# Optimization experiments

Measured on AMD Instinct MI355X. Metric: run time of the kernel, lower is better.

The kernel has to match this reference:

```python
import jax, jax.numpy as jnp
from jax import lax
import numpy as np

B, N = 8, 8192
NPOINT, RADIUS, NSAMPLE = 2048, 0.4, 64
EPS = 1e-5


def setup_inputs() -> dict:
    key = jax.random.key(0)
    ks = jax.random.split(key, 8)
    d = {
        'xyz': jax.random.normal(ks[0], (B, N, 3), jnp.float32),
        'features': jax.random.normal(ks[1], (B, 64, N), jnp.float32),
        'W0': jax.random.normal(ks[2], (64, 67), jnp.float32) * 0.1,
        'g0': jnp.ones((64,), jnp.float32), 'b0': jnp.zeros((64,), jnp.float32),
        'm0': jnp.zeros((64,), jnp.float32), 'v0': jnp.ones((64,), jnp.float32),
        'W1': jax.random.normal(ks[3], (64, 64), jnp.float32) * 0.1,
        'g1': jnp.ones((64,), jnp.float32), 'b1': jnp.zeros((64,), jnp.float32),
        'm1': jnp.zeros((64,), jnp.float32), 'v1': jnp.ones((64,), jnp.float32),
        'W2': jax.random.normal(ks[4], (128, 64), jnp.float32) * 0.1,
        'g2': jnp.ones((128,), jnp.float32), 'b2': jnp.zeros((128,), jnp.float32),
        'm2': jnp.zeros((128,), jnp.float32), 'v2': jnp.ones((128,), jnp.float32),
    }
    return d


def fps(xyz, npoint):
    # sequential furthest point sampling, start at index 0 (as in CUDA op)
    b = xyz.shape[0]
    first = jnp.zeros((b,), jnp.int32)
    d0 = jnp.sum((xyz - xyz[:, :1]) ** 2, -1)  # (B,N) dist to point 0

    def body(dist, _):
        nxt = jnp.argmax(dist, -1).astype(jnp.int32)
        p = jnp.take_along_axis(xyz, nxt[:, None, None].astype(jnp.int32), axis=1)
        dist = jnp.minimum(dist, jnp.sum((xyz - p) ** 2, -1))
        return dist, nxt

    _, rest = lax.scan(body, d0, None, length=npoint - 1)  # rest: (npoint-1, B)
    return jnp.concatenate([first[:, None], rest.T], axis=1)  # (B, npoint)


def ball_query(xyz, new_xyz, radius, nsample):
    # (B,P,N) squared distances
    d2 = jnp.sum((new_xyz[:, :, None, :] - xyz[:, None, :, :]) ** 2, -1)
    mask = d2 < radius * radius
    # stable sort: in-radius indices first, in original order (matches CUDA fill order)
    order = jnp.argsort(jnp.where(mask, 0, 1).astype(jnp.int32), axis=-1, stable=True)
    idx = order[..., :nsample]
    cnt = jnp.sum(mask, -1)  # (B,P)
    pos = jnp.arange(nsample)
    return jnp.where(pos < cnt[..., None], idx, idx[..., :1])  # pad with first found


def group(x, idx):
    # x (B,N,D), idx (B,P,S) -> (B,P,S,D)
    return jnp.take_along_axis(x[:, None], idx[..., None], axis=2)


def reference(xyz, features, W0, g0, b0, m0, v0, W1, g1, b1, m1, v1, W2, g2, b2, m2, v2):
    inds = fps(xyz, NPOINT)                                   # (B,P)
    new_xyz = jnp.take_along_axis(xyz, inds[..., None], axis=1)  # (B,P,3)
    idx = ball_query(xyz, new_xyz, RADIUS, NSAMPLE)           # (B,P,S)
    gxyz = group(xyz, idx) - new_xyz[:, :, None, :]           # (B,P,S,3) centered
    gfeat = group(jnp.swapaxes(features, 1, 2), idx)          # (B,P,S,C)
    x = jnp.concatenate([gxyz, gfeat], -1)                    # use_xyz concat
    x = jnp.transpose(x, (0, 3, 1, 2))                        # (B,C+3,P,S)
    for W, g, b, m, v in ((W0, g0, b0, m0, v0), (W1, g1, b1, m1, v1), (W2, g2, b2, m2, v2)):
        x = jnp.einsum('oi,bips->bops', W, x)                 # 1x1 conv
        scale = g / jnp.sqrt(v + EPS)
        x = (x - m[:, None, None]) * scale[:, None, None] + b[:, None, None]
        x = jax.nn.relu(x)
    new_features = jnp.max(x, -1)                             # max pool over nsample -> (B,128,P)
    return new_xyz, new_features, inds
```

## Files before the change

### kernel.cpp

```cpp
#include <hip/hip_runtime.h>
#include <cstdint>
#include <cstddef>

#define BATCH   8
#define NPTS    8192
#define NPOINT  2048
#define NSAMPLE 64
#define K0      67
#define C2      128

__device__ __forceinline__ float d2e(float ax, float ay, float az,
                                     float bx, float by, float bz) {
#pragma clang fp contract(off)
  float dx = ax - bx;
  float dy = ay - by;
  float dz = az - bz;
  float t0 = dx * dx;
  float t1 = dy * dy;
  float t2 = dz * dz;
  return (t0 + t1) + t2;
}

__device__ __forceinline__ float dpp_max_f32(float x) {
  int v;
  v = __builtin_amdgcn_update_dpp(__float_as_int(x), __float_as_int(x), 0xB1, 0xF, 0xF, false);
  x = fmaxf(x, __int_as_float(v));
  v = __builtin_amdgcn_update_dpp(__float_as_int(x), __float_as_int(x), 0x4E, 0xF, 0xF, false);
  x = fmaxf(x, __int_as_float(v));
  v = __builtin_amdgcn_update_dpp(__float_as_int(x), __float_as_int(x), 0x141, 0xF, 0xF, false);
  x = fmaxf(x, __int_as_float(v));
  v = __builtin_amdgcn_update_dpp(__float_as_int(x), __float_as_int(x), 0x140, 0xF, 0xF, false);
  x = fmaxf(x, __int_as_float(v));
  v = __builtin_amdgcn_update_dpp(__float_as_int(x), __float_as_int(x), 0x142, 0xA, 0xF, false);
  x = fmaxf(x, __int_as_float(v));
  v = __builtin_amdgcn_update_dpp(__float_as_int(x), __float_as_int(x), 0x143, 0xC, 0xF, false);
  x = fmaxf(x, __int_as_float(v));
  return __int_as_float(__builtin_amdgcn_readlane(__float_as_int(x), 63));
}

__device__ __forceinline__ int dpp_min_i32(int x) {
  int v;
  v = __builtin_amdgcn_update_dpp(x, x, 0xB1, 0xF, 0xF, false); x = min(x, v);
  v = __builtin_amdgcn_update_dpp(x, x, 0x4E, 0xF, 0xF, false); x = min(x, v);
  v = __builtin_amdgcn_update_dpp(x, x, 0x141, 0xF, 0xF, false); x = min(x, v);
  v = __builtin_amdgcn_update_dpp(x, x, 0x140, 0xF, 0xF, false); x = min(x, v);
  v = __builtin_amdgcn_update_dpp(x, x, 0x142, 0xA, 0xF, false); x = min(x, v);
  v = __builtin_amdgcn_update_dpp(x, x, 0x143, 0xC, 0xF, false); x = min(x, v);
  return __builtin_amdgcn_readlane(x, 63);
}

__global__ __launch_bounds__(512) void fps_kernel(const float* __restrict__ xyz,
                                                  float* __restrict__ out_xyz,
                                                  float* __restrict__ out_inds) {
  const int b = blockIdx.x;
  const int tid = threadIdx.x;
  const int lane = tid & 63, w = tid >> 6;

  __shared__ float2 sxy[NPTS];
  __shared__ float  szl[NPTS];
  __shared__ unsigned short sslot[NPOINT];
  __shared__ unsigned long long wred[2][8] __attribute__((aligned(16)));

  const float* xb = xyz + (size_t)b * NPTS * 3;

  for (int k = 0; k < 16; k++) {
    int i = tid + k * 512;
    sxy[i] = make_float2(xb[i * 3 + 0], xb[i * 3 + 1]);
    szl[i] = xb[i * 3 + 2];
  }
  __syncthreads();

  const float2 q0xy = sxy[0];
  const float q0x = q0xy.x, q0y = q0xy.y, q0z = szl[0];

  const int base = tid * 16;
  float px[16], py[16], pz[16], dd[16];
#pragma unroll
  for (int j = 0; j < 16; j++) {
    float2 xy = sxy[base + j];
    px[j] = xy.x; py[j] = xy.y; pz[j] = szl[base + j];
    dd[j] = d2e(px[j], py[j], pz[j], q0x, q0y, q0z);
  }
  if (tid == 0) sslot[0] = 0;

  {
    float bv = dd[0]; int bj = base;
#pragma unroll
    for (int j = 1; j < 16; j++) {
      bool better = dd[j] > bv;
      bv = better ? dd[j] : bv;
      bj = better ? base + j : bj;
    }
    float vm = dpp_max_f32(bv);
    int ci = (bv == vm) ? bj : 0x7FFFFFFF;
    int widx = dpp_min_i32(ci);
    if (lane == 0)
      wred[0][w] = ((unsigned long long)(~__float_as_uint(vm)) << 32) | (unsigned)widx;
  }
  __syncthreads();

  for (int t = 1; t < NPOINT; ++t) {
    const ulonglong2* wv = (const ulonglong2*)wred[(t - 1) & 1];
    ulonglong2 p0 = wv[0], p1 = wv[1], p2 = wv[2], p3 = wv[3];
    unsigned long long g0 = (p0.y < p0.x) ? p0.y : p0.x;
    unsigned long long g1 = (p1.y < p1.x) ? p1.y : p1.x;
    unsigned long long g2 = (p2.y < p2.x) ? p2.y : p2.x;
    unsigned long long g3 = (p3.y < p3.x) ? p3.y : p3.x;
    g0 = (g1 < g0) ? g1 : g0; g2 = (g3 < g2) ? g3 : g2;
    g0 = (g2 < g0) ? g2 : g0;
    const int nxt = (int)(g0 & 0xFFFFFFFFu);
    const float2 qxy = sxy[nxt];
    const float qx = qxy.x, qy = qxy.y, qz = szl[nxt];
    if (tid == 0) sslot[t] = (unsigned short)nxt;

    float d0 = d2e(px[0], py[0], pz[0], qx, qy, qz);
    dd[0] = fminf(dd[0], d0);
    float bv = dd[0]; int bj = base;
#pragma unroll
    for (int j = 1; j < 16; j++) {
      float d = d2e(px[j], py[j], pz[j], qx, qy, qz);
      dd[j] = fminf(dd[j], d);
      bool better = dd[j] > bv;
      bv = better ? dd[j] : bv;
      bj = better ? base + j : bj;
    }
    float vm = dpp_max_f32(bv);
    int ci = (bv == vm) ? bj : 0x7FFFFFFF;
    int widx = dpp_min_i32(ci);
    if (lane == 0)
      wred[t & 1][w] = ((unsigned long long)(~__float_as_uint(vm)) << 32) | (unsigned)widx;
    __syncthreads();
  }

  for (int t = tid; t < NPOINT; t += 512) {
    int o = (int)sslot[t];
    float2 xy = sxy[o];
    out_inds[b * NPOINT + t] = (float)o;
    out_xyz[((size_t)b * NPOINT + t) * 3 + 0] = xy.x;
    out_xyz[((size_t)b * NPOINT + t) * 3 + 1] = xy.y;
    out_xyz[((size_t)b * NPOINT + t) * 3 + 2] = szl[o];
  }
}

__global__ __launch_bounds__(128) void prep_kernel(
    const float* __restrict__ W0, const float* __restrict__ g0,
    const float* __restrict__ b0, const float* __restrict__ m0,
    const float* __restrict__ v0, const float* __restrict__ g1,
    const float* __restrict__ b1, const float* __restrict__ m1,
    const float* __restrict__ v1, const float* __restrict__ g2,
    const float* __restrict__ b2, const float* __restrict__ m2,
    const float* __restrict__ v2, float* __restrict__ wsp) {
  const int tid = threadIdx.x;
  if (tid < 64) {
    float s0 = g0[tid] / sqrtf(v0[tid] + 1e-5f);
    wsp[4 * tid + 0] = s0 * W0[tid * K0 + 0];
    wsp[4 * tid + 1] = s0 * W0[tid * K0 + 1];
    wsp[4 * tid + 2] = s0 * W0[tid * K0 + 2];
    wsp[4 * tid + 3] = b0[tid] - m0[tid] * s0;
    wsp[640 + tid] = s0;
    float s1 = g1[tid] / sqrtf(v1[tid] + 1e-5f);
    wsp[256 + tid] = s1; wsp[320 + tid] = b1[tid] - m1[tid] * s1;
  }
  float s2 = g2[tid] / sqrtf(v2[tid] + 1e-5f);
  wsp[384 + tid] = s2; wsp[512 + tid] = b2[tid] - m2[tid] * s2;
}

__global__ __launch_bounds__(256) void zfeat_kernel(const float* __restrict__ xyz,
                                                    const float* __restrict__ feat,
                                                    const float* __restrict__ W0,
                                                    const float* __restrict__ wsp,
                                                    float* __restrict__ szp) {
  __shared__ float ftile[64][64];
  __shared__ float sxyz[192];
  const int bt = blockIdx.x;
  const int b = bt >> 7, nt = bt & 127;
  const int tid = threadIdx.x;
  const int lane = tid & 63, w = tid >> 6;

  const float* fb = feat + (size_t)b * 64 * NPTS + (size_t)nt * 64;
#pragma unroll
  for (int r = w; r < 64; r += 4)
    ftile[r][lane] = fb[(size_t)r * NPTS + lane];
  if (tid < 192)
    sxyz[tid] = xyz[((size_t)b * NPTS + (size_t)nt * 64) * 3 + tid];

  float w0x = W0[lane * K0 + 0], w0y = W0[lane * K0 + 1], w0z = W0[lane * K0 + 2];
  float wf[64];
#pragma unroll
  for (int i = 0; i < 64; i++) wf[i] = W0[lane * K0 + 3 + i];
  const float s0 = wsp[640 + lane];
  __syncthreads();

  float* ob = szp + ((size_t)b * NPTS + (size_t)nt * 64) * 64;
  for (int u = w; u < 64; u += 4) {
    float acc = w0x * sxyz[u * 3 + 0] + w0y * sxyz[u * 3 + 1] + w0z * sxyz[u * 3 + 2];
#pragma unroll
    for (int i = 0; i < 64; i++) acc = fmaf(wf[i], ftile[i][u], acc);
    ob[(size_t)u * 64 + lane] = acc * s0;
  }
}

__global__ __launch_bounds__(256) void ballq_kernel(const float* __restrict__ xyz,
                                                    const float* __restrict__ new_xyz,
                                                    int* __restrict__ ball) {
  const int lane = threadIdx.x & 63;
  const int q = blockIdx.x * 4 + (threadIdx.x >> 6);
  const int b = q >> 11;
  const float RR = (float)(0.4 * 0.4);
  const float cx = new_xyz[(size_t)q * 3 + 0];
  const float cy = new_xyz[(size_t)q * 3 + 1];
  const float cz = new_xyz[(size_t)q * 3 + 2];
  const float* xb = xyz + (size_t)b * NPTS * 3;
  int cnt = 0, firsti = -1;
  for (int base = 0; base < NPTS; base += 64) {
    int i = base + lane;
    float xx = xb[i * 3 + 0], yy = xb[i * 3 + 1], zz = xb[i * 3 + 2];
    float d2 = d2e(xx, yy, zz, cx, cy, cz);
    bool m = d2 < RR;
    unsigned long long mask = __ballot(m);
    if (mask) {
      if (firsti < 0) firsti = base + (__ffsll((unsigned long long)mask) - 1);
      int pos = cnt + (int)__popcll(mask & ((1ull << lane) - 1ull));
      if (m && pos < NSAMPLE) ball[(size_t)q * NSAMPLE + pos] = i;
      cnt += (int)__popcll(mask);
      if (cnt >= NSAMPLE) break;
    }
  }
  for (int s = cnt + lane; s < NSAMPLE; s += 64)
    ball[(size_t)q * NSAMPLE + s] = firsti;
}

#define QPW 4
__global__ __launch_bounds__(256, 2) void mlp_kernel(
    const float* __restrict__ szp, const int* __restrict__ ball,
    const float* __restrict__ new_xyz, const float* __restrict__ W1,
    const float* __restrict__ W2, const float* __restrict__ wsp,
    float* __restrict__ out_feat) {
  __shared__ float ylds[4][2][64];
  __shared__ int   blds[4][64];
  const int tid = threadIdx.x;
  const int lane = tid & 63, wid = tid >> 6;

  float4 w1v[16], w2av[16], w2bv[16];
  const float4* W1r = (const float4*)(W1 + lane * 64);
  const float4* W2ar = (const float4*)(W2 + lane * 64);
  const float4* W2br = (const float4*)(W2 + (lane + 64) * 64);
#pragma unroll
  for (int i = 0; i < 16; i++) { w1v[i] = W1r[i]; w2av[i] = W2ar[i]; w2bv[i] = W2br[i]; }
  const float4 A = ((const float4*)wsp)[lane];
  const float sc1l = wsp[256 + lane], sh1l = wsp[320 + lane];
  const float sc2al = wsp[384 + lane], sh2al = wsp[512 + lane];
  const float sc2bl = wsp[448 + lane], sh2bl = wsp[576 + lane];

  float* yA = ylds[wid][0];
  float* yB = ylds[wid][1];
  const float4* yva = (const float4*)yA;
  const float4* yvb = (const float4*)yB;

  for (int qi = 0; qi < QPW; qi++) {
    const int q = blockIdx.x * (4 * QPW) + qi * 4 + wid;
    const int b = q >> 11, p = q & 2047;

    const float cx = new_xyz[(size_t)q * 3 + 0];
    const float cy = new_xyz[(size_t)q * 3 + 1];
    const float cz = new_xyz[(size_t)q * 3 + 2];
    const float hc = A.w - (A.x * cx + A.y * cy + A.z * cz);

    blds[wid][lane] = ball[(size_t)q * NSAMPLE + lane];
    const float* szb = szp + (size_t)b * NPTS * 64;
    __builtin_amdgcn_s_waitcnt(0);

    float vA = 0.f, vB = 0.f;
    int i0 = blds[wid][0], i1 = blds[wid][1];
    float fA = szb[(size_t)i0 * 64 + lane];
    float fB = szb[(size_t)i1 * 64 + lane];

    for (int s = 0; s < NSAMPLE; s += 2) {
      int sn0 = (s + 2 < NSAMPLE) ? s + 2 : s;
      int sn1 = (s + 3 < NSAMPLE) ? s + 3 : s;
      int in0 = blds[wid][sn0], in1 = blds[wid][sn1];
      float fn0 = szb[(size_t)in0 * 64 + lane];
      float fn1 = szb[(size_t)in1 * 64 + lane];

      float y0a = fmaxf(fA + hc, 0.f);
      float y0b = fmaxf(fB + hc, 0.f);
      yA[lane] = y0a;
      yB[lane] = y0b;
      float a0 = 0.f, a1 = 0.f, b0_ = 0.f, b1_ = 0.f;
#pragma unroll
      for (int i = 0; i < 16; i++) {
        float4 ya = yva[i], yb = yvb[i];
        float4 wv = w1v[i];
        a0 = fmaf(wv.x, ya.x, a0); a1 = fmaf(wv.y, ya.y, a1);
        a0 = fmaf(wv.z, ya.z, a0); a1 = fmaf(wv.w, ya.w, a1);
        b0_ = fmaf(wv.x, yb.x, b0_); b1_ = fmaf(wv.y, yb.y, b1_);
        b0_ = fmaf(wv.z, yb.z, b0_); b1_ = fmaf(wv.w, yb.w, b1_);
      }
      float y1a = fmaxf(fmaf(a0 + a1, sc1l, sh1l), 0.f);
      float y1b = fmaxf(fmaf(b0_ + b1_, sc1l, sh1l), 0.f);
      yA[lane] = y1a;
      yB[lane] = y1b;
      float c0 = 0.f, c1 = 0.f, e0 = 0.f, e1 = 0.f;
      float c0b = 0.f, c1b = 0.f, e0b = 0.f, e1b = 0.f;
#pragma unroll
      for (int i = 0; i < 16; i++) {
        float4 ya = yva[i], yb = yvb[i];
        float4 wa = w2av[i], wb = w2bv[i];
        c0 = fmaf(wa.x, ya.x, c0); c1 = fmaf(wa.y, ya.y, c1);
        c0 = fmaf(wa.z, ya.z, c0); c1 = fmaf(wa.w, ya.w, c1);
        e0 = fmaf(wb.x, ya.x, e0); e1 = fmaf(wb.y, ya.y, e1);
        e0 = fmaf(wb.z, ya.z, e0); e1 = fmaf(wb.w, ya.w, e1);
        c0b = fmaf(wa.x, yb.x, c0b); c1b = fmaf(wa.y, yb.y, c1b);
        c0b = fmaf(wa.z, yb.z, c0b); c1b = fmaf(wa.w, yb.w, c1b);
        e0b = fmaf(wb.x, yb.x, e0b); e1b = fmaf(wb.y, yb.y, e1b);
        e0b = fmaf(wb.z, yb.z, e0b); e1b = fmaf(wb.w, yb.w, e1b);
      }
      float y2aA = fmaxf(fmaf(c0 + c1, sc2al, sh2al), 0.f);
      float y2bA = fmaxf(fmaf(e0 + e1, sc2bl, sh2bl), 0.f);
      float y2aB = fmaxf(fmaf(c0b + c1b, sc2al, sh2al), 0.f);
      float y2bB = fmaxf(fmaf(e0b + e1b, sc2bl, sh2bl), 0.f);
      vA = fmaxf(vA, fmaxf(y2aA, y2aB));
      vB = fmaxf(vB, fmaxf(y2bA, y2bB));
      fA = fn0;
      fB = fn1;
    }
    out_feat[((size_t)b * C2 + lane) * NPOINT + p] = vA;
    out_feat[((size_t)b * C2 + lane + 64) * NPOINT + p] = vB;
  }
}

extern "C" void kernel_launch(void* const* d_in, const int* in_sizes, int n_in,
                              void* d_out, int out_size, void* d_ws, size_t ws_size,
                              hipStream_t stream) {
  const float* xyz  = (const float*)d_in[0];
  const float* feat = (const float*)d_in[1];
  const float* W0 = (const float*)d_in[2];
  const float* g0 = (const float*)d_in[3];
  const float* b0 = (const float*)d_in[4];
  const float* m0 = (const float*)d_in[5];
  const float* v0 = (const float*)d_in[6];
  const float* W1 = (const float*)d_in[7];
  const float* g1 = (const float*)d_in[8];
  const float* b1 = (const float*)d_in[9];
  const float* m1 = (const float*)d_in[10];
  const float* v1 = (const float*)d_in[11];
  const float* W2 = (const float*)d_in[12];
  const float* g2 = (const float*)d_in[13];
  const float* b2 = (const float*)d_in[14];
  const float* m2 = (const float*)d_in[15];
  const float* v2 = (const float*)d_in[16];

  float* out = (float*)d_out;
  float* out_xyz  = out;
  float* out_feat = out + 49152;
  float* out_inds = out + 49152 + 2097152;

  int*   ball = (int*)d_ws;
  float* szp  = (float*)((char*)d_ws + 4194304);
  float* wsp  = (float*)((char*)d_ws + 20971520);

  hipLaunchKernelGGL(prep_kernel, dim3(1), dim3(128), 0, stream,
                     W0, g0, b0, m0, v0, g1, b1, m1, v1, g2, b2, m2, v2, wsp);
  hipLaunchKernelGGL(zfeat_kernel, dim3(BATCH * (NPTS / 64)), dim3(256), 0, stream,
                     xyz, feat, W0, wsp, szp);
  hipLaunchKernelGGL(fps_kernel, dim3(BATCH), dim3(512), 0, stream,
                     xyz, out_xyz, out_inds);
  hipLaunchKernelGGL(ballq_kernel, dim3((BATCH * NPOINT) / 4), dim3(256), 0, stream,
                     xyz, out_xyz, ball);
  hipLaunchKernelGGL(mlp_kernel, dim3((BATCH * NPOINT) / (4 * QPW)), dim3(256), 0, stream,
                     szp, ball, out_xyz, W1, W2, wsp, out_feat);
}
```

Measured before the change: 2.714 ms.

## Fuse FPS, feature projection, ball query and MLP into one persistent streaming kernel

```diff
diff --git a/kernel.cpp b/kernel.cpp
--- a/kernel.cpp
+++ b/kernel.cpp
@@ -49,96 +49,265 @@
   return __builtin_amdgcn_readlane(x, 63);
 }
 
-__global__ __launch_bounds__(512) void fps_kernel(const float* __restrict__ xyz,
-                                                  float* __restrict__ out_xyz,
-                                                  float* __restrict__ out_inds) {
-  const int b = blockIdx.x;
+__device__ __forceinline__ void st_rel(int* p, int v) {
+  __hip_atomic_store(p, v, __ATOMIC_RELEASE, __HIP_MEMORY_SCOPE_AGENT);
+}
+__device__ __forceinline__ int ld_acq(int* p) {
+  return __hip_atomic_load(p, __ATOMIC_ACQUIRE, __HIP_MEMORY_SCOPE_AGENT);
+}
+
+__global__ __launch_bounds__(512, 2) void mega_kernel(
+    const float* __restrict__ xyz, const float* __restrict__ feat,
+    const float* __restrict__ W0, const float* __restrict__ W1,
+    const float* __restrict__ W2, const float* __restrict__ wsp,
+    float* __restrict__ szp, int* __restrict__ ctr,
+    float* __restrict__ out_xyz, float* __restrict__ out_feat,
+    float* __restrict__ out_inds) {
   const int tid = threadIdx.x;
-  const int lane = tid & 63, w = tid >> 6;
-
-  __shared__ float2 sxy[NPTS];
-  __shared__ float  szl[NPTS];
-  __shared__ unsigned short sslot[NPOINT];
-  __shared__ unsigned long long wred[2][8] __attribute__((aligned(16)));
-
-  const float* xb = xyz + (size_t)b * NPTS * 3;
-
-  for (int k = 0; k < 16; k++) {
-    int i = tid + k * 512;
-    sxy[i] = make_float2(xb[i * 3 + 0], xb[i * 3 + 1]);
-    szl[i] = xb[i * 3 + 2];
+  const int lane = tid & 63;
+  int* prog = ctr;
+  int* zcnt = ctr + 8;
+
+  if (blockIdx.x < 8) {
+    const int b = blockIdx.x;
+    const int w = tid >> 6;
+    __shared__ float2 sxy[NPTS];
+    __shared__ float  szl[NPTS];
+    __shared__ unsigned long long wred[2][8] __attribute__((aligned(16)));
+
+    const float* xb = xyz + (size_t)b * NPTS * 3;
+    for (int k = 0; k < 16; k++) {
+      int i = tid + k * 512;
+      sxy[i] = make_float2(xb[i * 3 + 0], xb[i * 3 + 1]);
+      szl[i] = xb[i * 3 + 2];
+    }
+    __syncthreads();
+
+    const float2 q0xy = sxy[0];
+    const float q0x = q0xy.x, q0y = q0xy.y, q0z = szl[0];
+
+    const int base = tid * 16;
+    float px[16], py[16], pz[16], dd[16];
+#pragma unroll
+    for (int j = 0; j < 16; j++) {
+      float2 xy = sxy[base + j];
+      px[j] = xy.x; py[j] = xy.y; pz[j] = szl[base + j];
+      dd[j] = d2e(px[j], py[j], pz[j], q0x, q0y, q0z);
+    }
+    if (tid == 0) {
+      out_inds[b * NPOINT] = 0.f;
+      out_xyz[(size_t)b * NPOINT * 3 + 0] = q0x;
+      out_xyz[(size_t)b * NPOINT * 3 + 1] = q0y;
+      out_xyz[(size_t)b * NPOINT * 3 + 2] = q0z;
+    }
+    {
+      float bv = dd[0]; int bj = base;
+#pragma unroll
+      for (int j = 1; j < 16; j++) {
+        bool better = dd[j] > bv;
+        bv = better ? dd[j] : bv;
+        bj = better ? base + j : bj;
+      }
+      float vm = dpp_max_f32(bv);
+      int ci = (bv == vm) ? bj : 0x7FFFFFFF;
+      int widx = dpp_min_i32(ci);
+      if (lane == 0)
+        wred[0][w] = ((unsigned long long)(~__float_as_uint(vm)) << 32) | (unsigned)widx;
+    }
+    __syncthreads();
+
+    for (int t = 1; t < NPOINT; ++t) {
+      const ulonglong2* wv = (const ulonglong2*)wred[(t - 1) & 1];
+      ulonglong2 p0 = wv[0], p1 = wv[1], p2 = wv[2], p3 = wv[3];
+      unsigned long long g0 = (p0.y < p0.x) ? p0.y : p0.x;
+      unsigned long long g1 = (p1.y < p1.x) ? p1.y : p1.x;
+      unsigned long long g2 = (p2.y < p2.x) ? p2.y : p2.x;
+      unsigned long long g3 = (p3.y < p3.x) ? p3.y : p3.x;
+      g0 = (g1 < g0) ? g1 : g0; g2 = (g3 < g2) ? g3 : g2;
+      g0 = (g2 < g0) ? g2 : g0;
+      const int nxt = (int)(g0 & 0xFFFFFFFFu);
+      const float2 qxy = sxy[nxt];
+      const float qx = qxy.x, qy = qxy.y, qz = szl[nxt];
+      if (tid == 0) {
+        out_inds[b * NPOINT + t] = (float)nxt;
+        out_xyz[((size_t)b * NPOINT + t) * 3 + 0] = qx;
+        out_xyz[((size_t)b * NPOINT + t) * 3 + 1] = qy;
+        out_xyz[((size_t)b * NPOINT + t) * 3 + 2] = qz;
+        if ((t & 31) == 31) st_rel(&prog[b], t + 1);
+      }
+
+      float d0 = d2e(px[0], py[0], pz[0], qx, qy, qz);
+      dd[0] = fminf(dd[0], d0);
+      float bv = dd[0]; int bj = base;
+#pragma unroll
+      for (int j = 1; j < 16; j++) {
+        float d = d2e(px[j], py[j], pz[j], qx, qy, qz);
+        dd[j] = fminf(dd[j], d);
+        bool better = dd[j] > bv;
+        bv = better ? dd[j] : bv;
+        bj = better ? base + j : bj;
+      }
+      float vm = dpp_max_f32(bv);
+      int ci = (bv == vm) ? bj : 0x7FFFFFFF;
+      int widx = dpp_min_i32(ci);
+      if (lane == 0)
+        wred[t & 1][w] = ((unsigned long long)(~__float_as_uint(vm)) << 32) | (unsigned)widx;
+      __syncthreads();
+    }
+    return;
+  }
+
+  const int wb = blockIdx.x - 8;
+  const int w8 = tid >> 6;
+  __shared__ float ftile[64][64];
+  __shared__ float sxyzt[192];
+  __shared__ float ylds2[8][2][64];
+  __shared__ int   blds8[8][64];
+
+  for (int tt = 0; tt < 2; tt++) {
+    const int bt = wb * 2 + tt;
+    const int B = bt >> 7, nt = bt & 127;
+    const float* fb = feat + (size_t)B * 64 * NPTS + (size_t)nt * 64;
+    for (int r = w8; r < 64; r += 8)
+      ftile[r][lane] = fb[(size_t)r * NPTS + lane];
+    if (tid < 192)
+      sxyzt[tid] = xyz[((size_t)B * NPTS + (size_t)nt * 64) * 3 + tid];
+    float w0x = W0[lane * K0 + 0], w0y = W0[lane * K0 + 1], w0z = W0[lane * K0 + 2];
+    float wf[64];
+#pragma unroll
+    for (int i = 0; i < 64; i++) wf[i] = W0[lane * K0 + 3 + i];
+    const float s0 = wsp[640 + lane];
+    __syncthreads();
+    float* ob = szp + ((size_t)B * NPTS + (size_t)nt * 64) * 64;
+    for (int u = w8; u < 64; u += 8) {
+      float acc = w0x * sxyzt[u * 3 + 0] + w0y * sxyzt[u * 3 + 1] + w0z * sxyzt[u * 3 + 2];
+#pragma unroll
+      for (int i = 0; i < 64; i++) acc = fmaf(wf[i], ftile[i][u], acc);
+      ob[(size_t)u * 64 + lane] = acc * s0;
+    }
+    __syncthreads();
+    if (tid == 0) {
+      __threadfence();
+      __hip_atomic_fetch_add(&zcnt[B], 1, __ATOMIC_RELEASE, __HIP_MEMORY_SCOPE_AGENT);
+    }
+  }
+
+  const int B0 = wb >> 6;
+  {
+    int guard = 0;
+    while (ld_acq(&zcnt[B0]) < 128 && ++guard < (1 << 20))
+      __builtin_amdgcn_s_sleep(8);
   }
   __syncthreads();
 
-  const float2 q0xy = sxy[0];
-  const float q0x = q0xy.x, q0y = q0xy.y, q0z = szl[0];
-
-  const int base = tid * 16;
-  float px[16], py[16], pz[16], dd[16];
-#pragma unroll
-  for (int j = 0; j < 16; j++) {
-    float2 xy = sxy[base + j];
-    px[j] = xy.x; py[j] = xy.y; pz[j] = szl[base + j];
-    dd[j] = d2e(px[j], py[j], pz[j], q0x, q0y, q0z);
-  }
-  if (tid == 0) sslot[0] = 0;
-
-  {
-    float bv = dd[0]; int bj = base;
-#pragma unroll
-    for (int j = 1; j < 16; j++) {
-      bool better = dd[j] > bv;
-      bv = better ? dd[j] : bv;
-      bj = better ? base + j : bj;
-    }
-    float vm = dpp_max_f32(bv);
-    int ci = (bv == vm) ? bj : 0x7FFFFFFF;
-    int widx = dpp_min_i32(ci);
-    if (lane == 0)
-      wred[0][w] = ((unsigned long long)(~__float_as_uint(vm)) << 32) | (unsigned)widx;
-  }
-  __syncthreads();
-
-  for (int t = 1; t < NPOINT; ++t) {
-    const ulonglong2* wv = (const ulonglong2*)wred[(t - 1) & 1];
-    ulonglong2 p0 = wv[0], p1 = wv[1], p2 = wv[2], p3 = wv[3];
-    unsigned long long g0 = (p0.y < p0.x) ? p0.y : p0.x;
-    unsigned long long g1 = (p1.y < p1.x) ? p1.y : p1.x;
-    unsigned long long g2 = (p2.y < p2.x) ? p2.y : p2.x;
-    unsigned long long g3 = (p3.y < p3.x) ? p3.y : p3.x;
-    g0 = (g1 < g0) ? g1 : g0; g2 = (g3 < g2) ? g3 : g2;
-    g0 = (g2 < g0) ? g2 : g0;
-    const int nxt = (int)(g0 & 0xFFFFFFFFu);
-    const float2 qxy = sxy[nxt];
-    const float qx = qxy.x, qy = qxy.y, qz = szl[nxt];
-    if (tid == 0) sslot[t] = (unsigned short)nxt;
-
-    float d0 = d2e(px[0], py[0], pz[0], qx, qy, qz);
-    dd[0] = fminf(dd[0], d0);
-    float bv = dd[0]; int bj = base;
-#pragma unroll
-    for (int j = 1; j < 16; j++) {
-      float d = d2e(px[j], py[j], pz[j], qx, qy, qz);
-      dd[j] = fminf(dd[j], d);
-      bool better = dd[j] > bv;
-      bv = better ? dd[j] : bv;
-      bj = better ? base + j : bj;
-    }
-    float vm = dpp_max_f32(bv);
-    int ci = (bv == vm) ? bj : 0x7FFFFFFF;
-    int widx = dpp_min_i32(ci);
-    if (lane == 0)
-      wred[t & 1][w] = ((unsigned long long)(~__float_as_uint(vm)) << 32) | (unsigned)widx;
-    __syncthreads();
-  }
-
-  for (int t = tid; t < NPOINT; t += 512) {
-    int o = (int)sslot[t];
-    float2 xy = sxy[o];
-    out_inds[b * NPOINT + t] = (float)o;
-    out_xyz[((size_t)b * NPOINT + t) * 3 + 0] = xy.x;
-    out_xyz[((size_t)b * NPOINT + t) * 3 + 1] = xy.y;
-    out_xyz[((size_t)b * NPOINT + t) * 3 + 2] = szl[o];
+  float4 w1v[16], w2av[16], w2bv[16];
+  const float4* W1r = (const float4*)(W1 + lane * 64);
+  const float4* W2ar = (const float4*)(W2 + lane * 64);
+  const float4* W2br = (const float4*)(W2 + (lane + 64) * 64);
+#pragma unroll
+  for (int i = 0; i < 16; i++) { w1v[i] = W1r[i]; w2av[i] = W2ar[i]; w2bv[i] = W2br[i]; }
+  const float4 Aq = ((const float4*)wsp)[lane];
+  const float sc1l = wsp[256 + lane], sh1l = wsp[320 + lane];
+  const float sc2al = wsp[384 + lane], sh2al = wsp[512 + lane];
+  const float sc2bl = wsp[448 + lane], sh2bl = wsp[576 + lane];
+  const float RR = (float)(0.4 * 0.4);
+
+  float* yA = ylds2[w8][0];
+  float* yB = ylds2[w8][1];
+  const float4* yva = (const float4*)yA;
+  const float4* yvb = (const float4*)yB;
+  int* bl = blds8[w8];
+  const float* xb = xyz + (size_t)B0 * NPTS * 3;
+  const float* szb = szp + (size_t)B0 * NPTS * 64;
+
+  for (int qi = 0; qi < 4; qi++) {
+    const int q = wb * 32 + qi * 8 + w8;
+    const int p = q & 2047;
+
+    {
+      int guard = 0;
+      while (ld_acq(&prog[B0]) < p + 1 && ++guard < (1 << 20))
+        __builtin_amdgcn_s_sleep(8);
+    }
+    const float cx = out_xyz[(size_t)q * 3 + 0];
+    const float cy = out_xyz[(size_t)q * 3 + 1];
+    const float cz = out_xyz[(size_t)q * 3 + 2];
+    const float hc = Aq.w - (Aq.x * cx + Aq.y * cy + Aq.z * cz);
+
+    int cnt = 0, firsti = -1;
+    for (int base2 = 0; base2 < NPTS; base2 += 64) {
+      int i = base2 + lane;
+      float xx = xb[i * 3 + 0], yy = xb[i * 3 + 1], zz = xb[i * 3 + 2];
+      float dq = d2e(xx, yy, zz, cx, cy, cz);
+      bool m = dq < RR;
+      unsigned long long mask = __ballot(m);
+      if (mask) {
+        if (firsti < 0) firsti = base2 + (__ffsll((unsigned long long)mask) - 1);
+        int pos = cnt + (int)__popcll(mask & ((1ull << lane) - 1ull));
+        if (m && pos < NSAMPLE) bl[pos] = i;
+        cnt += (int)__popcll(mask);
+        if (cnt >= NSAMPLE) break;
+      }
+    }
+    for (int s = cnt + lane; s < NSAMPLE; s += 64) bl[s] = firsti;
+    __builtin_amdgcn_s_waitcnt(0);
+
+    float vA = 0.f, vB = 0.f;
+    int i0 = bl[0], i1 = bl[1];
+    float fA = szb[(size_t)i0 * 64 + lane];
+    float fB = szb[(size_t)i1 * 64 + lane];
+
+    for (int s = 0; s < NSAMPLE; s += 2) {
+      int sn0 = (s + 2 < NSAMPLE) ? s + 2 : s;
+      int sn1 = (s + 3 < NSAMPLE) ? s + 3 : s;
+      int in0 = bl[sn0], in1 = bl[sn1];
+      float fn0 = szb[(size_t)in0 * 64 + lane];
+      float fn1 = szb[(size_t)in1 * 64 + lane];
+
+      float y0a = fmaxf(fA + hc, 0.f);
+      float y0b = fmaxf(fB + hc, 0.f);
+      yA[lane] = y0a;
+      yB[lane] = y0b;
+      float a0 = 0.f, a1 = 0.f, b0_ = 0.f, b1_ = 0.f;
+#pragma unroll
+      for (int i = 0; i < 16; i++) {
+        float4 ya = yva[i], yb = yvb[i];
+        float4 wv = w1v[i];
+        a0 = fmaf(wv.x, ya.x, a0); a1 = fmaf(wv.y, ya.y, a1);
+        a0 = fmaf(wv.z, ya.z, a0); a1 = fmaf(wv.w, ya.w, a1);
+        b0_ = fmaf(wv.x, yb.x, b0_); b1_ = fmaf(wv.y, yb.y, b1_);
+        b0_ = fmaf(wv.z, yb.z, b0_); b1_ = fmaf(wv.w, yb.w, b1_);
+      }
+      float y1a = fmaxf(fmaf(a0 + a1, sc1l, sh1l), 0.f);
+      float y1b = fmaxf(fmaf(b0_ + b1_, sc1l, sh1l), 0.f);
+      yA[lane] = y1a;
+      yB[lane] = y1b;
+      float c0 = 0.f, c1 = 0.f, e0 = 0.f, e1 = 0.f;
+      float c0b = 0.f, c1b = 0.f, e0b = 0.f, e1b = 0.f;
+#pragma unroll
+      for (int i = 0; i < 16; i++) {
+        float4 ya = yva[i], yb = yvb[i];
+        float4 wa = w2av[i], wbv = w2bv[i];
+        c0 = fmaf(wa.x, ya.x, c0); c1 = fmaf(wa.y, ya.y, c1);
+        c0 = fmaf(wa.z, ya.z, c0); c1 = fmaf(wa.w, ya.w, c1);
+        e0 = fmaf(wbv.x, ya.x, e0); e1 = fmaf(wbv.y, ya.y, e1);
+        e0 = fmaf(wbv.z, ya.z, e0); e1 = fmaf(wbv.w, ya.w, e1);
+        c0b = fmaf(wa.x, yb.x, c0b); c1b = fmaf(wa.y, yb.y, c1b);
+        c0b = fmaf(wa.z, yb.z, c0b); c1b = fmaf(wa.w, yb.w, c1b);
+        e0b = fmaf(wbv.x, yb.x, e0b); e1b = fmaf(wbv.y, yb.y, e1b);
+        e0b = fmaf(wbv.z, yb.z, e0b); e1b = fmaf(wbv.w, yb.w, e1b);
+      }
+      float y2aA = fmaxf(fmaf(c0 + c1, sc2al, sh2al), 0.f);
+      float y2bA = fmaxf(fmaf(e0 + e1, sc2bl, sh2bl), 0.f);
+      float y2aB = fmaxf(fmaf(c0b + c1b, sc2al, sh2al), 0.f);
+      float y2bB = fmaxf(fmaf(e0b + e1b, sc2bl, sh2bl), 0.f);
+      vA = fmaxf(vA, fmaxf(y2aA, y2aB));
+      vB = fmaxf(vB, fmaxf(y2bA, y2bB));
+      fA = fn0;
+      fB = fn1;
+    }
+    out_feat[((size_t)B0 * C2 + lane) * NPOINT + p] = vA;
+    out_feat[((size_t)B0 * C2 + lane + 64) * NPOINT + p] = vB;
   }
 }
 
@@ -149,8 +318,10 @@
     const float* __restrict__ b1, const float* __restrict__ m1,
     const float* __restrict__ v1, const float* __restrict__ g2,
     const float* __restrict__ b2, const float* __restrict__ m2,
-    const float* __restrict__ v2, float* __restrict__ wsp) {
+    const float* __restrict__ v2, float* __restrict__ wsp,
+    int* __restrict__ ctr) {
   const int tid = threadIdx.x;
+  if (tid < 16) ctr[tid] = 0;
   if (tid < 64) {
     float s0 = g0[tid] / sqrtf(v0[tid] + 1e-5f);
     wsp[4 * tid + 0] = s0 * W0[tid * K0 + 0];
@@ -163,170 +334,6 @@
   }
   float s2 = g2[tid] / sqrtf(v2[tid] + 1e-5f);
   wsp[384 + tid] = s2; wsp[512 + tid] = b2[tid] - m2[tid] * s2;
-}
-
-__global__ __launch_bounds__(256) void zfeat_kernel(const float* __restrict__ xyz,
-                                                    const float* __restrict__ feat,
-                                                    const float* __restrict__ W0,
-                                                    const float* __restrict__ wsp,
-                                                    float* __restrict__ szp) {
-  __shared__ float ftile[64][64];
-  __shared__ float sxyz[192];
-  const int bt = blockIdx.x;
-  const int b = bt >> 7, nt = bt & 127;
-  const int tid = threadIdx.x;
-  const int lane = tid & 63, w = tid >> 6;
-
-  const float* fb = feat + (size_t)b * 64 * NPTS + (size_t)nt * 64;
-#pragma unroll
-  for (int r = w; r < 64; r += 4)
-    ftile[r][lane] = fb[(size_t)r * NPTS + lane];
-  if (tid < 192)
-    sxyz[tid] = xyz[((size_t)b * NPTS + (size_t)nt * 64) * 3 + tid];
-
-  float w0x = W0[lane * K0 + 0], w0y = W0[lane * K0 + 1], w0z = W0[lane * K0 + 2];
-  float wf[64];
-#pragma unroll
-  for (int i = 0; i < 64; i++) wf[i] = W0[lane * K0 + 3 + i];
-  const float s0 = wsp[640 + lane];
-  __syncthreads();
-
-  float* ob = szp + ((size_t)b * NPTS + (size_t)nt * 64) * 64;
-  for (int u = w; u < 64; u += 4) {
-    float acc = w0x * sxyz[u * 3 + 0] + w0y * sxyz[u * 3 + 1] + w0z * sxyz[u * 3 + 2];
-#pragma unroll
-    for (int i = 0; i < 64; i++) acc = fmaf(wf[i], ftile[i][u], acc);
-    ob[(size_t)u * 64 + lane] = acc * s0;
-  }
-}
-
-__global__ __launch_bounds__(256) void ballq_kernel(const float* __restrict__ xyz,
-                                                    const float* __restrict__ new_xyz,
-                                                    int* __restrict__ ball) {
-  const int lane = threadIdx.x & 63;
-  const int q = blockIdx.x * 4 + (threadIdx.x >> 6);
-  const int b = q >> 11;
-  const float RR = (float)(0.4 * 0.4);
-  const float cx = new_xyz[(size_t)q * 3 + 0];
-  const float cy = new_xyz[(size_t)q * 3 + 1];
-  const float cz = new_xyz[(size_t)q * 3 + 2];
-  const float* xb = xyz + (size_t)b * NPTS * 3;
-  int cnt = 0, firsti = -1;
-  for (int base = 0; base < NPTS; base += 64) {
-    int i = base + lane;
-    float xx = xb[i * 3 + 0], yy = xb[i * 3 + 1], zz = xb[i * 3 + 2];
-    float d2 = d2e(xx, yy, zz, cx, cy, cz);
-    bool m = d2 < RR;
-    unsigned long long mask = __ballot(m);
-    if (mask) {
-      if (firsti < 0) firsti = base + (__ffsll((unsigned long long)mask) - 1);
-      int pos = cnt + (int)__popcll(mask & ((1ull << lane) - 1ull));
-      if (m && pos < NSAMPLE) ball[(size_t)q * NSAMPLE + pos] = i;
-      cnt += (int)__popcll(mask);
-      if (cnt >= NSAMPLE) break;
-    }
-  }
-  for (int s = cnt + lane; s < NSAMPLE; s += 64)
-    ball[(size_t)q * NSAMPLE + s] = firsti;
-}
-
-#define QPW 4
-__global__ __launch_bounds__(256, 2) void mlp_kernel(
-    const float* __restrict__ szp, const int* __restrict__ ball,
-    const float* __restrict__ new_xyz, const float* __restrict__ W1,
-    const float* __restrict__ W2, const float* __restrict__ wsp,
-    float* __restrict__ out_feat) {
-  __shared__ float ylds[4][2][64];
-  __shared__ int   blds[4][64];
-  const int tid = threadIdx.x;
-  const int lane = tid & 63, wid = tid >> 6;
-
-  float4 w1v[16], w2av[16], w2bv[16];
-  const float4* W1r = (const float4*)(W1 + lane * 64);
-  const float4* W2ar = (const float4*)(W2 + lane * 64);
-  const float4* W2br = (const float4*)(W2 + (lane + 64) * 64);
-#pragma unroll
-  for (int i = 0; i < 16; i++) { w1v[i] = W1r[i]; w2av[i] = W2ar[i]; w2bv[i] = W2br[i]; }
-  const float4 A = ((const float4*)wsp)[lane];
-  const float sc1l = wsp[256 + lane], sh1l = wsp[320 + lane];
-  const float sc2al = wsp[384 + lane], sh2al = wsp[512 + lane];
-  const float sc2bl = wsp[448 + lane], sh2bl = wsp[576 + lane];
-
-  float* yA = ylds[wid][0];
-  float* yB = ylds[wid][1];
-  const float4* yva = (const float4*)yA;
-  const float4* yvb = (const float4*)yB;
-
-  for (int qi = 0; qi < QPW; qi++) {
-    const int q = blockIdx.x * (4 * QPW) + qi * 4 + wid;
-    const int b = q >> 11, p = q & 2047;
-
-    const float cx = new_xyz[(size_t)q * 3 + 0];
-    const float cy = new_xyz[(size_t)q * 3 + 1];
-    const float cz = new_xyz[(size_t)q * 3 + 2];
-    const float hc = A.w - (A.x * cx + A.y * cy + A.z * cz);
-
-    blds[wid][lane] = ball[(size_t)q * NSAMPLE + lane];
-    const float* szb = szp + (size_t)b * NPTS * 64;
-    __builtin_amdgcn_s_waitcnt(0);
-
-    float vA = 0.f, vB = 0.f;
-    int i0 = blds[wid][0], i1 = blds[wid][1];
-    float fA = szb[(size_t)i0 * 64 + lane];
-    float fB = szb[(size_t)i1 * 64 + lane];
-
-    for (int s = 0; s < NSAMPLE; s += 2) {
-      int sn0 = (s + 2 < NSAMPLE) ? s + 2 : s;
-      int sn1 = (s + 3 < NSAMPLE) ? s + 3 : s;
-      int in0 = blds[wid][sn0], in1 = blds[wid][sn1];
-      float fn0 = szb[(size_t)in0 * 64 + lane];
-      float fn1 = szb[(size_t)in1 * 64 + lane];
-
-      float y0a = fmaxf(fA + hc, 0.f);
-      float y0b = fmaxf(fB + hc, 0.f);
-      yA[lane] = y0a;
-      yB[lane] = y0b;
-      float a0 = 0.f, a1 = 0.f, b0_ = 0.f, b1_ = 0.f;
-#pragma unroll
-      for (int i = 0; i < 16; i++) {
-        float4 ya = yva[i], yb = yvb[i];
-        float4 wv = w1v[i];
-        a0 = fmaf(wv.x, ya.x, a0); a1 = fmaf(wv.y, ya.y, a1);
-        a0 = fmaf(wv.z, ya.z, a0); a1 = fmaf(wv.w, ya.w, a1);
-        b0_ = fmaf(wv.x, yb.x, b0_); b1_ = fmaf(wv.y, yb.y, b1_);
-        b0_ = fmaf(wv.z, yb.z, b0_); b1_ = fmaf(wv.w, yb.w, b1_);
-      }
-      float y1a = fmaxf(fmaf(a0 + a1, sc1l, sh1l), 0.f);
-      float y1b = fmaxf(fmaf(b0_ + b1_, sc1l, sh1l), 0.f);
-      yA[lane] = y1a;
-      yB[lane] = y1b;
-      float c0 = 0.f, c1 = 0.f, e0 = 0.f, e1 = 0.f;
-      float c0b = 0.f, c1b = 0.f, e0b = 0.f, e1b = 0.f;
-#pragma unroll
-      for (int i = 0; i < 16; i++) {
-        float4 ya = yva[i], yb = yvb[i];
-        float4 wa = w2av[i], wb = w2bv[i];
-        c0 = fmaf(wa.x, ya.x, c0); c1 = fmaf(wa.y, ya.y, c1);
-        c0 = fmaf(wa.z, ya.z, c0); c1 = fmaf(wa.w, ya.w, c1);
-        e0 = fmaf(wb.x, ya.x, e0); e1 = fmaf(wb.y, ya.y, e1);
-        e0 = fmaf(wb.z, ya.z, e0); e1 = fmaf(wb.w, ya.w, e1);
-        c0b = fmaf(wa.x, yb.x, c0b); c1b = fmaf(wa.y, yb.y, c1b);
-        c0b = fmaf(wa.z, yb.z, c0b); c1b = fmaf(wa.w, yb.w, c1b);
-        e0b = fmaf(wb.x, yb.x, e0b); e1b = fmaf(wb.y, yb.y, e1b);
-        e0b = fmaf(wb.z, yb.z, e0b); e1b = fmaf(wb.w, yb.w, e1b);
-      }
-      float y2aA = fmaxf(fmaf(c0 + c1, sc2al, sh2al), 0.f);
-      float y2bA = fmaxf(fmaf(e0 + e1, sc2bl, sh2bl), 0.f);
-      float y2aB = fmaxf(fmaf(c0b + c1b, sc2al, sh2al), 0.f);
-      float y2bB = fmaxf(fmaf(e0b + e1b, sc2bl, sh2bl), 0.f);
-      vA = fmaxf(vA, fmaxf(y2aA, y2aB));
-      vB = fmaxf(vB, fmaxf(y2bA, y2bB));
-      fA = fn0;
-      fB = fn1;
-    }
-    out_feat[((size_t)b * C2 + lane) * NPOINT + p] = vA;
-    out_feat[((size_t)b * C2 + lane + 64) * NPOINT + p] = vB;
-  }
 }
 
 extern "C" void kernel_launch(void* const* d_in, const int* in_sizes, int n_in,
@@ -355,18 +362,14 @@
   float* out_feat = out + 49152;
   float* out_inds = out + 49152 + 2097152;
 
-  int*   ball = (int*)d_ws;
-  float* szp  = (float*)((char*)d_ws + 4194304);
-  float* wsp  = (float*)((char*)d_ws + 20971520);
+  float* szp = (float*)d_ws;
+  float* wsp = (float*)((char*)d_ws + 20971520);
+  int*   ctr = (int*)((char*)d_ws + 20975616);
 
   hipLaunchKernelGGL(prep_kernel, dim3(1), dim3(128), 0, stream,
-                     W0, g0, b0, m0, v0, g1, b1, m1, v1, g2, b2, m2, v2, wsp);
-  hipLaunchKernelGGL(zfeat_kernel, dim3(BATCH * (NPTS / 64)), dim3(256), 0, stream,
-                     xyz, feat, W0, wsp, szp);
-  hipLaunchKernelGGL(fps_kernel, dim3(BATCH), dim3(512), 0, stream,
-                     xyz, out_xyz, out_inds);
-  hipLaunchKernelGGL(ballq_kernel, dim3((BATCH * NPOINT) / 4), dim3(256), 0, stream,
-                     xyz, out_xyz, ball);
-  hipLaunchKernelGGL(mlp_kernel, dim3((BATCH * NPOINT) / (4 * QPW)), dim3(256), 0, stream,
-                     szp, ball, out_xyz, W1, W2, wsp, out_feat);
-}
+                     W0, g0, b0, m0, v0, g1, b1, m1, v1, g2, b2, m2, v2,
+                     wsp, ctr);
+  hipLaunchKernelGGL(mega_kernel, dim3(8 + 512), dim3(512), 0, stream,
+                     xyz, feat, W0, W1, W2, wsp, szp, ctr,
+                     out_xyz, out_feat, out_inds);
+}
```

Result: slower. 2.871 ms (+5.8%).
